# Kernel tuning notes

Hardware: AMD Instinct MI355X
Metric: run time of the kernel (lower is better)

The kernel has to match this reference:

```python
import jax, jax.numpy as jnp
import numpy as np
import math

B, S, E, H = 8, 1024, 512, 8
EPS = 1e-5

def _ln(x, g, b):
    mu = jnp.mean(x, axis=-1, keepdims=True)
    var = jnp.mean(jnp.square(x - mu), axis=-1, keepdims=True)
    return (x - mu) * jax.lax.rsqrt(var + EPS) * g + b

def setup_inputs() -> dict:
    key = jax.random.key(0)
    ks = iter(jax.random.split(key, 40))
    def w(shape, scale=0.02):
        return jax.random.normal(next(ks), shape, dtype=jnp.float32) * scale
    inp = {
        'x': jax.random.normal(next(ks), (B, S, E), dtype=jnp.float32),
        'cond': jax.random.normal(next(ks), (B, 1, E), dtype=jnp.float32),
        # AdaLN modulation linears (stored as (in,out))
        'g1w': w((E, E)), 'g1b': jnp.zeros((E,), jnp.float32),
        'be1w': w((E, E)), 'be1b': jnp.zeros((E,), jnp.float32),
        'a1w': w((E, E)), 'a1b': jnp.zeros((E,), jnp.float32),
        'g2w': w((E, E)), 'g2b': jnp.zeros((E,), jnp.float32),
        'be2w': w((E, E)), 'be2b': jnp.zeros((E,), jnp.float32),
        'a2w': w((E, E)), 'a2b': jnp.zeros((E,), jnp.float32),
        # LayerNorm affine
        'ln1g': jnp.ones((E,), jnp.float32), 'ln1b': jnp.zeros((E,), jnp.float32),
        'ln2g': jnp.ones((E,), jnp.float32), 'ln2b': jnp.zeros((E,), jnp.float32),
        # attention projections: each head has width E -> out dim H*E
        'wq': w((E, H * E)), 'bq': jnp.zeros((H * E,), jnp.float32),
        'wk': w((E, H * E)), 'bk': jnp.zeros((H * E,), jnp.float32),
        'wv': w((E, H * E)), 'bv': jnp.zeros((H * E,), jnp.float32),
        'lvw': w((H * E, E)), 'lvb': jnp.zeros((E,), jnp.float32),
        # FFN
        'f1w': w((E, 4 * E)), 'f1b': jnp.zeros((4 * E,), jnp.float32),
        'f2w': w((4 * E, E)), 'f2b': jnp.zeros((E,), jnp.float32),
    }
    return inp

def reference(x, cond, g1w, g1b, be1w, be1b, a1w, a1b, g2w, g2b, be2w, be2b, a2w, a2b,
              ln1g, ln1b, ln2g, ln2b, wq, bq, wk, bk, wv, bv, lvw, lvb, f1w, f1b, f2w, f2b):
    # AdaLN modulation signals, each (B,1,E)
    gamma1 = cond @ g1w + g1b
    beta1 = cond @ be1w + be1b
    alpha1 = cond @ a1w + a1b
    gamma2 = cond @ g2w + g2b
    beta2 = cond @ be2w + be2b
    alpha2 = cond @ a2w + a2b

    y = _ln(x, ln1g, ln1b) * (1.0 + gamma1) + beta1
    q = (y @ wq + bq).reshape(B, S, H, E).transpose(0, 2, 1, 3)  # (B,H,S,E)
    k = (y @ wk + bk).reshape(B, S, H, E).transpose(0, 2, 1, 3)
    v = (y @ wv + bv).reshape(B, S, H, E).transpose(0, 2, 1, 3)
    # NOTE: original scales by sqrt(q.size(2)) == sqrt(seq_len), not head_dim
    scale = 1.0 / math.sqrt(S)
    attn = jax.nn.softmax(jnp.einsum('bhse,bhte->bhst', q, k) * scale, axis=-1)
    o = jnp.einsum('bhst,bhte->bhse', attn, v)  # (B,H,S,E)
    o = o.transpose(0, 2, 1, 3).reshape(B, S, H * E)
    y = x + (o @ lvw + lvb) * alpha1

    z = _ln(y, ln2g, ln2b) * (1.0 + gamma2) + beta2
    z = (jax.nn.relu(z @ f1w + f1b) @ f2w + f2b) * alpha2
    return y + z
```

## Files before the change

kernel.cpp:

```cpp
#include <hip/hip_runtime.h>
#include <hip/hip_bf16.h>

typedef __bf16 bf16_t;
typedef bf16_t bf16x8 __attribute__((ext_vector_type(8)));
typedef bf16_t bf16x4 __attribute__((ext_vector_type(4)));
typedef float f32x4 __attribute__((ext_vector_type(4)));

typedef const __attribute__((address_space(1))) void GV;
typedef __attribute__((address_space(3))) void LV;

__device__ __forceinline__ void gload_lds16(const bf16_t* gsrc, bf16_t* ldst) {
    __builtin_amdgcn_global_load_lds((GV*)gsrc, (LV*)ldst, 16, 0, 0);
}

__global__ __launch_bounds__(256) void wtrans_all_kernel(
    const float* __restrict__ wq, const float* __restrict__ wk, const float* __restrict__ wv,
    const float* __restrict__ lvw, const float* __restrict__ f1w, const float* __restrict__ f2w,
    bf16_t* __restrict__ wqT, bf16_t* __restrict__ lvwT,
    bf16_t* __restrict__ f1wT, bf16_t* __restrict__ f2wT)
{
    __shared__ float tile[32][33];
    const int bid = blockIdx.x;
    const float* in; bf16_t* out; int K, N, nx, local;
    if (bid < 6144) {
        const int sec = bid >> 11;
        local = bid & 2047;
        in = (sec == 0) ? wq : ((sec == 1) ? wk : wv);
        out = wqT + (long long)sec * 2097152;
        K = 512; N = 4096; nx = 128;
    } else if (bid < 8192) {
        local = bid - 6144; in = lvw; out = lvwT; K = 4096; N = 512; nx = 16;
    } else if (bid < 9216) {
        local = bid - 8192; in = f1w; out = f1wT; K = 512; N = 2048; nx = 64;
    } else {
        local = bid - 9216; in = f2w; out = f2wT; K = 2048; N = 512; nx = 16;
    }
    const int n0 = (local % nx) * 32, k0 = (local / nx) * 32;
    const int tx = threadIdx.x & 31, ty = threadIdx.x >> 5;
#pragma unroll
    for (int i = 0; i < 32; i += 8)
        tile[ty + i][tx] = in[(long long)(k0 + ty + i) * N + n0 + tx];
    __syncthreads();
#pragma unroll
    for (int i = 0; i < 32; i += 8)
        out[(long long)(n0 + ty + i) * K + k0 + tx] = (bf16_t)tile[tx][ty + i];
}

__global__ __launch_bounds__(256) void modsig_kernel(
    const float* __restrict__ cond,
    const float* __restrict__ w0, const float* __restrict__ w1, const float* __restrict__ w2,
    const float* __restrict__ w3, const float* __restrict__ w4, const float* __restrict__ w5,
    const float* __restrict__ c0, const float* __restrict__ c1, const float* __restrict__ c2,
    const float* __restrict__ c3, const float* __restrict__ c4, const float* __restrict__ c5,
    float* __restrict__ out)
{
    __shared__ float cs[512];
    const int sig = blockIdx.x >> 3, b = blockIdx.x & 7;
    const float* w; const float* bi;
    switch (sig) {
        case 0: w = w0; bi = c0; break;
        case 1: w = w1; bi = c1; break;
        case 2: w = w2; bi = c2; break;
        case 3: w = w3; bi = c3; break;
        case 4: w = w4; bi = c4; break;
        default: w = w5; bi = c5; break;
    }
    for (int i = threadIdx.x; i < 512; i += 256) cs[i] = cond[b * 512 + i];
    __syncthreads();
    for (int n = threadIdx.x; n < 512; n += 256) {
        float s0 = 0.f, s1 = 0.f, s2 = 0.f, s3 = 0.f;
        for (int i = 0; i < 512; i += 4) {
            s0 = fmaf(cs[i], w[(long long)i * 512 + n], s0);
            s1 = fmaf(cs[i + 1], w[(long long)(i + 1) * 512 + n], s1);
            s2 = fmaf(cs[i + 2], w[(long long)(i + 2) * 512 + n], s2);
            s3 = fmaf(cs[i + 3], w[(long long)(i + 3) * 512 + n], s3);
        }
        out[(long long)(sig * 8 + b) * 512 + n] = bi[n] + (s0 + s1) + (s2 + s3);
    }
}

__global__ __launch_bounds__(128) void ln_mod_kernel(
    const float* __restrict__ x, const float* __restrict__ g, const float* __restrict__ be,
    const float* __restrict__ gamma, const float* __restrict__ beta, bf16_t* __restrict__ out)
{
    const int row = blockIdx.x;
    const int b = row >> 10;
    const int t = threadIdx.x;
    const float4 v = reinterpret_cast<const float4*>(x + (long long)row * 512)[t];
    float s = v.x + v.y + v.z + v.w;
    float ss = v.x * v.x + v.y * v.y + v.z * v.z + v.w * v.w;
    for (int o = 32; o; o >>= 1) { s += __shfl_xor(s, o); ss += __shfl_xor(ss, o); }
    __shared__ float red[4];
    if ((t & 63) == 0) { red[t >> 6] = s; red[2 + (t >> 6)] = ss; }
    __syncthreads();
    s = red[0] + red[1]; ss = red[2] + red[3];
    const float mu = s * (1.f / 512.f);
    const float rstd = rsqrtf(ss * (1.f / 512.f) - mu * mu + 1e-5f);
    const float4 gv = reinterpret_cast<const float4*>(g)[t];
    const float4 bv = reinterpret_cast<const float4*>(be)[t];
    const float4 ga = reinterpret_cast<const float4*>(gamma + b * 512)[t];
    const float4 bb = reinterpret_cast<const float4*>(beta + b * 512)[t];
    bf16x4 ov;
    ov[0] = (bf16_t)(((v.x - mu) * rstd * gv.x + bv.x) * (1.f + ga.x) + bb.x);
    ov[1] = (bf16_t)(((v.y - mu) * rstd * gv.y + bv.y) * (1.f + ga.y) + bb.y);
    ov[2] = (bf16_t)(((v.z - mu) * rstd * gv.z + bv.z) * (1.f + ga.z) + bb.z);
    ov[3] = (bf16_t)(((v.w - mu) * rstd * gv.w + bv.w) * (1.f + ga.w) + bb.w);
    reinterpret_cast<bf16x4*>(out + (long long)row * 512)[t] = ov;
}

template <int EPI>
__global__ __launch_bounds__(256) void gemm128_kernel(
    const bf16_t* __restrict__ A, const bf16_t* __restrict__ B,
    const float* __restrict__ bias, void* Cout,
    int M, int N, int K, int lda, int ldb, int ldc)
{
    const int nbx = gridDim.x;
    const int lin = blockIdx.y * nbx + blockIdx.x;
    const int cpx = (nbx * gridDim.y) >> 3;
    const int swz = (lin & 7) * cpx + (lin >> 3);
    const int m0 = (swz / nbx) * 128, n0 = (swz % nbx) * 128;
    const int tid = threadIdx.x, lane = tid & 63, wid = tid >> 6;
    const int wr = wid >> 1, wc = wid & 1;

    __shared__ bf16_t As[16384];
    __shared__ bf16_t Bs[16384];

    f32x4 acc[4][4];
#pragma unroll
    for (int m = 0; m < 4; ++m)
#pragma unroll
        for (int n = 0; n < 4; ++n) acc[m][n] = (f32x4){0.f, 0.f, 0.f, 0.f};

    const int r8 = lane >> 3;
    const int lc = (lane & 7) ^ r8;
    long long aOff[4], bOff[4];
#pragma unroll
    for (int i = 0; i < 4; ++i) {
        const int row = i * 32 + wid * 8 + r8;
        aOff[i] = (long long)(m0 + row) * lda + lc * 8;
        bOff[i] = (long long)(n0 + row) * ldb + lc * 8;
    }

    const int frow = lane & 15, lg = lane >> 4;
    const int p0 = lg ^ (frow & 7);

#pragma unroll
    for (int i = 0; i < 4; ++i) gload_lds16(A + aOff[i], As + i * 2048 + wid * 512);
#pragma unroll
    for (int i = 0; i < 4; ++i) gload_lds16(B + bOff[i], Bs + i * 2048 + wid * 512);

    for (int kt = 0; kt < K; kt += 64) {
        const int cur = (kt >> 6) & 1;
        __syncthreads();
        if (kt + 64 < K) {
            const int nxt = (cur ^ 1) * 8192;
#pragma unroll
            for (int i = 0; i < 4; ++i) gload_lds16(A + aOff[i] + kt + 64, As + nxt + i * 2048 + wid * 512);
#pragma unroll
            for (int i = 0; i < 4; ++i) gload_lds16(B + bOff[i] + kt + 64, Bs + nxt + i * 2048 + wid * 512);
        }
        const bf16_t* Ab = As + cur * 8192;
        const bf16_t* Bb = Bs + cur * 8192;
        __builtin_amdgcn_s_setprio(1);
#pragma unroll
        for (int kk = 0; kk < 2; ++kk) {
            const int pc = p0 ^ (kk << 2);
            bf16x8 af[4], bfv[4];
#pragma unroll
            for (int m = 0; m < 4; ++m)
                af[m] = *reinterpret_cast<const bf16x8*>(Ab + (wr * 64 + m * 16 + frow) * 64 + pc * 8);
#pragma unroll
            for (int n = 0; n < 4; ++n)
                bfv[n] = *reinterpret_cast<const bf16x8*>(Bb + (wc * 64 + n * 16 + frow) * 64 + pc * 8);
#pragma unroll
            for (int m = 0; m < 4; ++m)
#pragma unroll
                for (int n = 0; n < 4; ++n)
                    acc[m][n] = __builtin_amdgcn_mfma_f32_16x16x32_bf16(af[m], bfv[n], acc[m][n], 0, 0, 0);
        }
        __builtin_amdgcn_s_setprio(0);
    }

#pragma unroll
    for (int m = 0; m < 4; ++m) {
        const int gm = m0 + wr * 64 + m * 16 + ((lane >> 4) << 2);
#pragma unroll
        for (int n = 0; n < 4; ++n) {
            const int gn = n0 + wc * 64 + n * 16 + (lane & 15);
            const float bb = bias ? bias[gn] : 0.f;
#pragma unroll
            for (int j = 0; j < 4; ++j) {
                const float v = acc[m][n][j] + bb;
                const int gmj = gm + j;
                if (EPI == 0) {
                    ((bf16_t*)Cout)[(long long)gmj * ldc + gn] = (bf16_t)v;
                } else {
                    ((bf16_t*)Cout)[(long long)gmj * ldc + gn] = (bf16_t)fmaxf(v, 0.f);
                }
            }
        }
    }
}

__global__ __launch_bounds__(256) void gemmqkv_kernel(
    const bf16_t* __restrict__ A, const bf16_t* __restrict__ B,
    const float* __restrict__ bq, const float* __restrict__ bk, const float* __restrict__ bv,
    bf16_t* __restrict__ qkv, bf16_t* __restrict__ vtb)
{
    const int lin = blockIdx.y * 96 + blockIdx.x;
    const int swz = (lin & 7) * 768 + (lin >> 3);
    const int m0 = (swz / 96) * 128, n0 = (swz % 96) * 128;
    const int sec = n0 >> 12;
    const float* bias = (sec == 0) ? bq : ((sec == 1) ? bk : bv);
    const int tid = threadIdx.x, lane = tid & 63, wid = tid >> 6;
    const int wr = wid >> 1, wc = wid & 1;

    __shared__ bf16_t As[16384];
    __shared__ bf16_t Bs[16384];

    f32x4 acc[4][4];
#pragma unroll
    for (int m = 0; m < 4; ++m)
#pragma unroll
        for (int n = 0; n < 4; ++n) acc[m][n] = (f32x4){0.f, 0.f, 0.f, 0.f};

    const int r8 = lane >> 3;
    const int lc = (lane & 7) ^ r8;
    long long aOff[4], bOff[4];
#pragma unroll
    for (int i = 0; i < 4; ++i) {
        const int row = i * 32 + wid * 8 + r8;
        aOff[i] = (long long)(m0 + row) * 512 + lc * 8;
        bOff[i] = (long long)(n0 + row) * 512 + lc * 8;
    }

    const int frow = lane & 15, lg = lane >> 4;
    const int p0 = lg ^ (frow & 7);

#pragma unroll
    for (int i = 0; i < 4; ++i) gload_lds16(A + aOff[i], As + i * 2048 + wid * 512);
#pragma unroll
    for (int i = 0; i < 4; ++i) gload_lds16(B + bOff[i], Bs + i * 2048 + wid * 512);

    for (int kt = 0; kt < 512; kt += 64) {
        const int cur = (kt >> 6) & 1;
        __syncthreads();
        if (kt + 64 < 512) {
            const int nxt = (cur ^ 1) * 8192;
#pragma unroll
            for (int i = 0; i < 4; ++i) gload_lds16(A + aOff[i] + kt + 64, As + nxt + i * 2048 + wid * 512);
#pragma unroll
            for (int i = 0; i < 4; ++i) gload_lds16(B + bOff[i] + kt + 64, Bs + nxt + i * 2048 + wid * 512);
        }
        const bf16_t* Ab = As + cur * 8192;
        const bf16_t* Bb = Bs + cur * 8192;
        __builtin_amdgcn_s_setprio(1);
#pragma unroll
        for (int kk = 0; kk < 2; ++kk) {
            const int pc = p0 ^ (kk << 2);
            bf16x8 af[4], bfv[4];
#pragma unroll
            for (int m = 0; m < 4; ++m)
                af[m] = *reinterpret_cast<const bf16x8*>(Ab + (wr * 64 + m * 16 + frow) * 64 + pc * 8);
#pragma unroll
            for (int n = 0; n < 4; ++n)
                bfv[n] = *reinterpret_cast<const bf16x8*>(Bb + (wc * 64 + n * 16 + frow) * 64 + pc * 8);
#pragma unroll
            for (int m = 0; m < 4; ++m)
#pragma unroll
                for (int n = 0; n < 4; ++n)
                    acc[m][n] = __builtin_amdgcn_mfma_f32_16x16x32_bf16(af[m], bfv[n], acc[m][n], 0, 0, 0);
        }
        __builtin_amdgcn_s_setprio(0);
    }

#pragma unroll
    for (int m = 0; m < 4; ++m) {
        const int gm = m0 + wr * 64 + m * 16 + ((lane >> 4) << 2);
#pragma unroll
        for (int n = 0; n < 4; ++n) {
            const int gn = n0 + wc * 64 + n * 16 + (lane & 15);
            const int gnl = gn & 4095;
            const float bb = bias[gnl];
#pragma unroll
            for (int j = 0; j < 4; ++j) {
                const float v = acc[m][n][j] + bb;
                const int gmj = gm + j;
                if (sec < 2) {
                    qkv[(long long)sec * 33554432 + (long long)gmj * 4096 + gnl] = (bf16_t)v;
                } else {
                    const long long ci =
                        (long long)(((gmj >> 10) * 8 + (gnl >> 9)) * 512 + (gnl & 511)) * 1024 + (gmj & 1023);
                    vtb[ci] = (bf16_t)v;
                }
            }
        }
    }
}

__global__ __launch_bounds__(256) void gemm64_kernel(
    const bf16_t* __restrict__ A, const bf16_t* __restrict__ B,
    const float* __restrict__ bias, float* __restrict__ Cout,
    const float* __restrict__ resid, const float* __restrict__ alpha,
    int M, int N, int K, int lda, int ldb)
{
    const int nbx = gridDim.x;
    const int lin = blockIdx.y * nbx + blockIdx.x;
    const int cpx = (nbx * gridDim.y) >> 3;
    const int swz = (lin & 7) * cpx + (lin >> 3);
    const int m0 = (swz / nbx) * 64, n0 = (swz % nbx) * 128;
    const int tid = threadIdx.x, lane = tid & 63, wid = tid >> 6;
    const int wr = wid >> 1, wc = wid & 1;

    __shared__ bf16_t As[8192];
    __shared__ bf16_t Bs[16384];

    f32x4 acc[2][4];
#pragma unroll
    for (int m = 0; m < 2; ++m)
#pragma unroll
        for (int n = 0; n < 4; ++n) acc[m][n] = (f32x4){0.f, 0.f, 0.f, 0.f};

    const int r8 = lane >> 3;
    const int lc = (lane & 7) ^ r8;
    long long aOff[2], bOff[4];
#pragma unroll
    for (int i = 0; i < 2; ++i)
        aOff[i] = (long long)(m0 + i * 32 + wid * 8 + r8) * lda + lc * 8;
#pragma unroll
    for (int i = 0; i < 4; ++i)
        bOff[i] = (long long)(n0 + i * 32 + wid * 8 + r8) * ldb + lc * 8;

    const int frow = lane & 15, lg = lane >> 4;
    const int p0 = lg ^ (frow & 7);

#pragma unroll
    for (int i = 0; i < 2; ++i) gload_lds16(A + aOff[i], As + i * 2048 + wid * 512);
#pragma unroll
    for (int i = 0; i < 4; ++i) gload_lds16(B + bOff[i], Bs + i * 2048 + wid * 512);

    for (int kt = 0; kt < K; kt += 64) {
        const int cur = (kt >> 6) & 1;
        __syncthreads();
        if (kt + 64 < K) {
#pragma unroll
            for (int i = 0; i < 2; ++i)
                gload_lds16(A + aOff[i] + kt + 64, As + (cur ^ 1) * 4096 + i * 2048 + wid * 512);
#pragma unroll
            for (int i = 0; i < 4; ++i)
                gload_lds16(B + bOff[i] + kt + 64, Bs + (cur ^ 1) * 8192 + i * 2048 + wid * 512);
        }
        const bf16_t* Ab = As + cur * 4096;
        const bf16_t* Bb = Bs + cur * 8192;
        __builtin_amdgcn_s_setprio(1);
#pragma unroll
        for (int kk = 0; kk < 2; ++kk) {
            const int pc = p0 ^ (kk << 2);
            bf16x8 af[2], bfv[4];
#pragma unroll
            for (int m = 0; m < 2; ++m)
                af[m] = *reinterpret_cast<const bf16x8*>(Ab + (wr * 32 + m * 16 + frow) * 64 + pc * 8);
#pragma unroll
            for (int n = 0; n < 4; ++n)
                bfv[n] = *reinterpret_cast<const bf16x8*>(Bb + (wc * 64 + n * 16 + frow) * 64 + pc * 8);
#pragma unroll
            for (int m = 0; m < 2; ++m)
#pragma unroll
                for (int n = 0; n < 4; ++n)
                    acc[m][n] = __builtin_amdgcn_mfma_f32_16x16x32_bf16(af[m], bfv[n], acc[m][n], 0, 0, 0);
        }
        __builtin_amdgcn_s_setprio(0);
    }

#pragma unroll
    for (int m = 0; m < 2; ++m) {
        const int gm = m0 + wr * 32 + m * 16 + ((lane >> 4) << 2);
#pragma unroll
        for (int n = 0; n < 4; ++n) {
            const int gn = n0 + wc * 64 + n * 16 + (lane & 15);
            const float bb = bias[gn];
#pragma unroll
            for (int j = 0; j < 4; ++j) {
                const int gmj = gm + j;
                const long long ci = (long long)gmj * 512 + gn;
                Cout[ci] = resid[ci] + (acc[m][n][j] + bb) * alpha[(gmj >> 10) * 512 + gn];
            }
        }
    }
}

#define FA_LDS 68608
#define SCL 0.04508422132207354f
__global__ __launch_bounds__(256, 2) void flash_kernel(
    bf16_t* __restrict__ qb, const bf16_t* __restrict__ kb, const bf16_t* __restrict__ vtb)
{
    extern __shared__ char smem[];
    bf16_t* Ks = (bf16_t*)smem;
    bf16_t* Vs = (bf16_t*)(smem + 32768);
    char* PB = smem + 65536;
    float* pmaxB = (float*)(smem + 67584);
    float* psumB = (float*)(smem + 68096);

    const int bid = blockIdx.x;
    const int xcd = bid & 7, idx = bid >> 3;
    const int qt = idx & 31, bhl = idx >> 5;
    const int bh = xcd * 8 + bhl;
    const int b = bh >> 3, h = bh & 7;
    const int q0 = qt * 32;
    const int tid = threadIdx.x, lane = tid & 63, wid = tid >> 6;
    const int laneq = lane & 15, lx = lane & 7, lg = lane >> 4;
    const int wk = wid >> 1, wq = wid & 1;
    const int we = wid;

#pragma unroll
    for (int r = 0; r < 8; ++r) {
        const int row = r * 4 + wid;
        gload_lds16(kb + ((long long)(b * 1024 + row) * 8 + h) * 512 + ((lane ^ (row & 7)) << 3),
                    Ks + row * 512);
    }
    const int qi = wq * 16 + laneq;
    bf16x8 qfrag[16];
    {
        const bf16_t* qrow = qb + ((long long)(b * 1024 + q0 + qi) * 8 + h) * 512 + lg * 8;
#pragma unroll
        for (int ks = 0; ks < 16; ++ks) qfrag[ks] = *reinterpret_cast<const bf16x8*>(qrow + ks * 32);
    }
    f32x4 accA[8], accB[8];
#pragma unroll
    for (int e = 0; e < 8; ++e) { accA[e] = (f32x4){0.f,0.f,0.f,0.f}; accB[e] = (f32x4){0.f,0.f,0.f,0.f}; }
    float mS = 0.f, mPA = 0.f, mPB = 0.f, lA = 0.f, lB = 0.f;
    const int rA = wk * 16 + laneq;
    const int qA = laneq, qB = laneq + 16;
    __syncthreads();

    for (int t = 0; t < 32; ++t) {
#pragma unroll
        for (int r = 0; r < 8; ++r) {
            const int e0 = (r * 4 + wid) * 16;
            const int e = e0 + (lane >> 2);
            gload_lds16(vtb + ((long long)bh * 512 + e) * 1024 + t * 32 + (((lane & 3) ^ (e & 3)) << 3),
                        Vs + e0 * 32);
        }
        f32x4 s0 = (f32x4){0.f, 0.f, 0.f, 0.f};
        const char* KsB = (const char*)Ks;
        __builtin_amdgcn_s_setprio(1);
#pragma unroll
        for (int ks = 0; ks < 16; ++ks) {
            const int co = (((ks * 4 + lg) ^ lx) << 4);
            bf16x8 a0 = *(const bf16x8*)(KsB + rA * 1024 + co);
            s0 = __builtin_amdgcn_mfma_f32_16x16x32_bf16(a0, qfrag[ks], s0, 0, 0, 0);
        }
        __builtin_amdgcn_s_setprio(0);
        float f[4], pe[4];
#pragma unroll
        for (int j = 0; j < 4; ++j) f[j] = s0[j] * SCL;
        float mloc = fmaxf(fmaxf(f[0], f[1]), fmaxf(f[2], f[3]));
        mloc = fmaxf(mloc, __shfl_xor(mloc, 16));
        mloc = fmaxf(mloc, __shfl_xor(mloc, 32));
        float sl = 0.f;
#pragma unroll
        for (int j = 0; j < 4; ++j) { pe[j] = exp2f(f[j] - mS); sl += pe[j]; }
        sl += __shfl_xor(sl, 16);
        sl += __shfl_xor(sl, 32);
        if (lane < 16) {
            pmaxB[(t & 1) * 64 + wk * 32 + wq * 16 + lane] = mloc;
            psumB[(t & 1) * 64 + wk * 32 + wq * 16 + lane] = sl;
        }
        {
            bf16x4 p;
#pragma unroll
            for (int j = 0; j < 4; ++j) p[j] = (bf16_t)pe[j];
            const int g = wk * 4 + lg;
            *(bf16x4*)(PB + qi * 64 + (((g >> 1) ^ (qi & 3)) << 4) + ((g & 1) << 3)) = p;
        }
        __syncthreads();

        if (t < 31) {
#pragma unroll
            for (int r = 0; r < 8; ++r) {
                const int row = r * 4 + wid;
                gload_lds16(kb + ((long long)(b * 1024 + t * 32 + 32 + row) * 8 + h) * 512
                                + ((lane ^ (row & 7)) << 3),
                            Ks + row * 512);
            }
        }
        const char* VB = (const char*)Vs;
        bf16x8 pA = *(const bf16x8*)(PB + qA * 64 + ((lg ^ (qA & 3)) << 4));
        bf16x8 pBv = *(const bf16x8*)(PB + qB * 64 + ((lg ^ (qB & 3)) << 4));
        __builtin_amdgcn_s_setprio(1);
#pragma unroll
        for (int ef = 0; ef < 8; ++ef) {
            const int re = we * 128 + ef * 16 + laneq;
            bf16x8 av = *(const bf16x8*)(VB + re * 64 + ((lg ^ (re & 3)) << 4));
            accA[ef] = __builtin_amdgcn_mfma_f32_16x16x32_bf16(av, pA, accA[ef], 0, 0, 0);
            accB[ef] = __builtin_amdgcn_mfma_f32_16x16x32_bf16(av, pBv, accB[ef], 0, 0, 0);
        }
        __builtin_amdgcn_s_setprio(0);
        {
            const float* pmax_t = pmaxB + (t & 1) * 64;
            const float* psum_t = psumB + (t & 1) * 64;
            mS = fmaxf(mS, fmaxf(pmax_t[qi], pmax_t[32 + qi]));
            lA += psum_t[qA] + psum_t[32 + qA];
            lB += psum_t[qB] + psum_t[32 + qB];
            const float mnA = fmaxf(mPA, fmaxf(pmax_t[qA], pmax_t[32 + qA]));
            const float mnB = fmaxf(mPB, fmaxf(pmax_t[qB], pmax_t[32 + qB]));
            if (__ballot((mnA > mPA) || (mnB > mPB))) {
                const float rsA = exp2f(mPA - mnA), rsB = exp2f(mPB - mnB);
                lA *= rsA; lB *= rsB;
#pragma unroll
                for (int e = 0; e < 8; ++e) {
#pragma unroll
                    for (int j = 0; j < 4; ++j) { accA[e][j] *= rsA; accB[e][j] *= rsB; }
                }
            }
            mPA = mnA; mPB = mnB;
        }
        __syncthreads();
    }

    const float iA = 1.f / lA, iB = 1.f / lB;
#pragma unroll
    for (int ef = 0; ef < 8; ++ef) {
        const int e0 = we * 128 + ef * 16 + lg * 4;
        bf16x4 oA, oB;
#pragma unroll
        for (int j = 0; j < 4; ++j) { oA[j] = (bf16_t)(accA[ef][j] * iA); oB[j] = (bf16_t)(accB[ef][j] * iB); }
        *(bf16x4*)(qb + ((long long)(b * 1024 + q0 + qA) * 8 + h) * 512 + e0) = oA;
        *(bf16x4*)(qb + ((long long)(b * 1024 + q0 + qB) * 8 + h) * 512 + e0) = oB;
    }
}

extern "C" void kernel_launch(void* const* d_in, const int* in_sizes, int n_in,
                              void* d_out, int out_size, void* d_ws, size_t ws_size,
                              hipStream_t stream)
{
    const float* x    = (const float*)d_in[0];
    const float* cond = (const float*)d_in[1];
    const float* g1w  = (const float*)d_in[2];  const float* g1b  = (const float*)d_in[3];
    const float* be1w = (const float*)d_in[4];  const float* be1b = (const float*)d_in[5];
    const float* a1w  = (const float*)d_in[6];  const float* a1b  = (const float*)d_in[7];
    const float* g2w  = (const float*)d_in[8];  const float* g2b  = (const float*)d_in[9];
    const float* be2w = (const float*)d_in[10]; const float* be2b = (const float*)d_in[11];
    const float* a2w  = (const float*)d_in[12]; const float* a2b  = (const float*)d_in[13];
    const float* ln1g = (const float*)d_in[14]; const float* ln1b = (const float*)d_in[15];
    const float* ln2g = (const float*)d_in[16]; const float* ln2b = (const float*)d_in[17];
    const float* wq   = (const float*)d_in[18]; const float* bq   = (const float*)d_in[19];
    const float* wk   = (const float*)d_in[20]; const float* bk   = (const float*)d_in[21];
    const float* wv   = (const float*)d_in[22]; const float* bv   = (const float*)d_in[23];
    const float* lvw  = (const float*)d_in[24]; const float* lvb  = (const float*)d_in[25];
    const float* f1w  = (const float*)d_in[26]; const float* f1b  = (const float*)d_in[27];
    const float* f2w  = (const float*)d_in[28]; const float* f2b  = (const float*)d_in[29];
    (void)in_sizes; (void)n_in; (void)out_size; (void)ws_size;

    char* w8 = (char*)d_ws;
    float*  mod  = (float*)(w8);
    bf16_t* wqT  = (bf16_t*)(w8 + 98304);
    bf16_t* lvwT = (bf16_t*)(w8 + 98304 + 3 * 4194304);
    bf16_t* f1wT = (bf16_t*)(w8 + 98304 + 4 * 4194304);
    bf16_t* f2wT = (bf16_t*)(w8 + 98304 + 4 * 4194304 + 2097152);
    bf16_t* ybf  = (bf16_t*)(w8 + 98304 + 4 * 4194304 + 2 * 2097152);
    bf16_t* qb   = (bf16_t*)(w8 + 98304 + 4 * 4194304 + 2 * 2097152 + 8388608);
    bf16_t* kb   = qb + 33554432;
    bf16_t* vtb  = kb + 33554432;

    (void)hipFuncSetAttribute((const void*)flash_kernel,
                              hipFuncAttributeMaxDynamicSharedMemorySize, FA_LDS);

    const dim3 blk(256);
    wtrans_all_kernel<<<10240, blk, 0, stream>>>(wq, wk, wv, lvw, f1w, f2w,
                                                 wqT, lvwT, f1wT, f2wT);
    modsig_kernel<<<48, blk, 0, stream>>>(cond, g1w, be1w, a1w, g2w, be2w, a2w,
                                          g1b, be1b, a1b, g2b, be2b, a2b, mod);
    ln_mod_kernel<<<8192, 128, 0, stream>>>(x, ln1g, ln1b, mod, mod + 4096, ybf);
    gemmqkv_kernel<<<dim3(96, 64), blk, 0, stream>>>(ybf, wqT, bq, bk, bv, qb, vtb);
    flash_kernel<<<2048, 256, FA_LDS, stream>>>(qb, kb, vtb);
    gemm64_kernel<<<dim3(4, 128), blk, 0, stream>>>(qb, lvwT, lvb, (float*)d_out, x, mod + 8192,
        8192, 512, 4096, 4096, 4096);
    ln_mod_kernel<<<8192, 128, 0, stream>>>((const float*)d_out, ln2g, ln2b,
                                            mod + 12288, mod + 16384, ybf);
    gemm128_kernel<1><<<dim3(16, 64), blk, 0, stream>>>(ybf, f1wT, f1b, qb,
        8192, 2048, 512, 512, 512, 2048);
    gemm64_kernel<<<dim3(4, 128), blk, 0, stream>>>(qb, f2wT, f2b, (float*)d_out,
        (const float*)d_out, mod + 20480,
        8192, 512, 2048, 2048, 2048);
}
```

Before: 678.9 us.

## Merge weight transpose and modulation kernels; reswizzle flash attention LDS layouts

Folds the AdaLN modulation-signal matmul into the weight-transpose kernel as 48 extra blocks, removing one launch. In the flash kernel it changes the XOR swizzle for the V and P tiles in LDS to key on (row>>1)&3 instead of row&3, to reduce bank conflicts on 64-byte rows. It also interleaves the per-row max and sum partials so each row's two partials are read with one float2 load. The partial buffers grow LDS use by 1 KB, which may affect occupancy at two blocks per CU.

```diff
diff --git a/kernel.cpp b/kernel.cpp
--- a/kernel.cpp
+++ b/kernel.cpp
@@ -13,69 +13,70 @@
     __builtin_amdgcn_global_load_lds((GV*)gsrc, (LV*)ldst, 16, 0, 0);
 }
 
-__global__ __launch_bounds__(256) void wtrans_all_kernel(
+__global__ __launch_bounds__(256) void prep_kernel(
     const float* __restrict__ wq, const float* __restrict__ wk, const float* __restrict__ wv,
     const float* __restrict__ lvw, const float* __restrict__ f1w, const float* __restrict__ f2w,
     bf16_t* __restrict__ wqT, bf16_t* __restrict__ lvwT,
-    bf16_t* __restrict__ f1wT, bf16_t* __restrict__ f2wT)
-{
-    __shared__ float tile[32][33];
+    bf16_t* __restrict__ f1wT, bf16_t* __restrict__ f2wT,
+    const float* __restrict__ cond,
+    const float* __restrict__ mw0, const float* __restrict__ mw1, const float* __restrict__ mw2,
+    const float* __restrict__ mw3, const float* __restrict__ mw4, const float* __restrict__ mw5,
+    const float* __restrict__ mc0, const float* __restrict__ mc1, const float* __restrict__ mc2,
+    const float* __restrict__ mc3, const float* __restrict__ mc4, const float* __restrict__ mc5,
+    float* __restrict__ mod)
+{
+    __shared__ float sbuf[32 * 33];
     const int bid = blockIdx.x;
-    const float* in; bf16_t* out; int K, N, nx, local;
-    if (bid < 6144) {
-        const int sec = bid >> 11;
-        local = bid & 2047;
-        in = (sec == 0) ? wq : ((sec == 1) ? wk : wv);
-        out = wqT + (long long)sec * 2097152;
-        K = 512; N = 4096; nx = 128;
-    } else if (bid < 8192) {
-        local = bid - 6144; in = lvw; out = lvwT; K = 4096; N = 512; nx = 16;
-    } else if (bid < 9216) {
-        local = bid - 8192; in = f1w; out = f1wT; K = 512; N = 2048; nx = 64;
+    if (bid < 10240) {
+        float (*tile)[33] = (float(*)[33])sbuf;
+        const float* in; bf16_t* out; int N, nx, K, local;
+        if (bid < 6144) {
+            const int sec = bid >> 11;
+            local = bid & 2047;
+            in = (sec == 0) ? wq : ((sec == 1) ? wk : wv);
+            out = wqT + (long long)sec * 2097152;
+            K = 512; N = 4096; nx = 128;
+        } else if (bid < 8192) {
+            local = bid - 6144; in = lvw; out = lvwT; K = 4096; N = 512; nx = 16;
+        } else if (bid < 9216) {
+            local = bid - 8192; in = f1w; out = f1wT; K = 512; N = 2048; nx = 64;
+        } else {
+            local = bid - 9216; in = f2w; out = f2wT; K = 2048; N = 512; nx = 16;
+        }
+        const int n0 = (local % nx) * 32, k0 = (local / nx) * 32;
+        const int tx = threadIdx.x & 31, ty = threadIdx.x >> 5;
+#pragma unroll
+        for (int i = 0; i < 32; i += 8)
+            tile[ty + i][tx] = in[(long long)(k0 + ty + i) * N + n0 + tx];
+        __syncthreads();
+#pragma unroll
+        for (int i = 0; i < 32; i += 8)
+            out[(long long)(n0 + ty + i) * K + k0 + tx] = (bf16_t)tile[tx][ty + i];
     } else {
-        local = bid - 9216; in = f2w; out = f2wT; K = 2048; N = 512; nx = 16;
-    }
-    const int n0 = (local % nx) * 32, k0 = (local / nx) * 32;
-    const int tx = threadIdx.x & 31, ty = threadIdx.x >> 5;
-#pragma unroll
-    for (int i = 0; i < 32; i += 8)
-        tile[ty + i][tx] = in[(long long)(k0 + ty + i) * N + n0 + tx];
-    __syncthreads();
-#pragma unroll
-    for (int i = 0; i < 32; i += 8)
-        out[(long long)(n0 + ty + i) * K + k0 + tx] = (bf16_t)tile[tx][ty + i];
-}
-
-__global__ __launch_bounds__(256) void modsig_kernel(
-    const float* __restrict__ cond,
-    const float* __restrict__ w0, const float* __restrict__ w1, const float* __restrict__ w2,
-    const float* __restrict__ w3, const float* __restrict__ w4, const float* __restrict__ w5,
-    const float* __restrict__ c0, const float* __restrict__ c1, const float* __restrict__ c2,
-    const float* __restrict__ c3, const float* __restrict__ c4, const float* __restrict__ c5,
-    float* __restrict__ out)
-{
-    __shared__ float cs[512];
-    const int sig = blockIdx.x >> 3, b = blockIdx.x & 7;
-    const float* w; const float* bi;
-    switch (sig) {
-        case 0: w = w0; bi = c0; break;
-        case 1: w = w1; bi = c1; break;
-        case 2: w = w2; bi = c2; break;
-        case 3: w = w3; bi = c3; break;
-        case 4: w = w4; bi = c4; break;
-        default: w = w5; bi = c5; break;
-    }
-    for (int i = threadIdx.x; i < 512; i += 256) cs[i] = cond[b * 512 + i];
-    __syncthreads();
-    for (int n = threadIdx.x; n < 512; n += 256) {
-        float s0 = 0.f, s1 = 0.f, s2 = 0.f, s3 = 0.f;
-        for (int i = 0; i < 512; i += 4) {
-            s0 = fmaf(cs[i], w[(long long)i * 512 + n], s0);
-            s1 = fmaf(cs[i + 1], w[(long long)(i + 1) * 512 + n], s1);
-            s2 = fmaf(cs[i + 2], w[(long long)(i + 2) * 512 + n], s2);
-            s3 = fmaf(cs[i + 3], w[(long long)(i + 3) * 512 + n], s3);
-        }
-        out[(long long)(sig * 8 + b) * 512 + n] = bi[n] + (s0 + s1) + (s2 + s3);
+        float* cs = sbuf;
+        const int lb = bid - 10240;
+        const int sig = lb >> 3, b = lb & 7;
+        const float* w; const float* bi;
+        switch (sig) {
+            case 0: w = mw0; bi = mc0; break;
+            case 1: w = mw1; bi = mc1; break;
+            case 2: w = mw2; bi = mc2; break;
+            case 3: w = mw3; bi = mc3; break;
+            case 4: w = mw4; bi = mc4; break;
+            default: w = mw5; bi = mc5; break;
+        }
+        for (int i = threadIdx.x; i < 512; i += 256) cs[i] = cond[b * 512 + i];
+        __syncthreads();
+        for (int n = threadIdx.x; n < 512; n += 256) {
+            float s0 = 0.f, s1 = 0.f, s2 = 0.f, s3 = 0.f;
+            for (int i = 0; i < 512; i += 4) {
+                s0 = fmaf(cs[i], w[(long long)i * 512 + n], s0);
+                s1 = fmaf(cs[i + 1], w[(long long)(i + 1) * 512 + n], s1);
+                s2 = fmaf(cs[i + 2], w[(long long)(i + 2) * 512 + n], s2);
+                s3 = fmaf(cs[i + 3], w[(long long)(i + 3) * 512 + n], s3);
+            }
+            mod[(long long)(sig * 8 + b) * 512 + n] = bi[n] + (s0 + s1) + (s2 + s3);
+        }
     }
 }
 
@@ -389,7 +390,7 @@
     }
 }
 
-#define FA_LDS 68608
+#define FA_LDS 69632
 #define SCL 0.04508422132207354f
 __global__ __launch_bounds__(256, 2) void flash_kernel(
     bf16_t* __restrict__ qb, const bf16_t* __restrict__ kb, const bf16_t* __restrict__ vtb)
@@ -399,7 +400,7 @@
     bf16_t* Vs = (bf16_t*)(smem + 32768);
     char* PB = smem + 65536;
     float* pmaxB = (float*)(smem + 67584);
-    float* psumB = (float*)(smem + 68096);
+    float* psumB = (float*)(smem + 68608);
 
     const int bid = blockIdx.x;
     const int xcd = bid & 7, idx = bid >> 3;
@@ -438,7 +439,8 @@
         for (int r = 0; r < 8; ++r) {
             const int e0 = (r * 4 + wid) * 16;
             const int e = e0 + (lane >> 2);
-            gload_lds16(vtb + ((long long)bh * 512 + e) * 1024 + t * 32 + (((lane & 3) ^ (e & 3)) << 3),
+            gload_lds16(vtb + ((long long)bh * 512 + e) * 1024 + t * 32
+                            + (((lane & 3) ^ ((e >> 1) & 3)) << 3),
                         Vs + e0 * 32);
         }
         f32x4 s0 = (f32x4){0.f, 0.f, 0.f, 0.f};
@@ -463,15 +465,16 @@
         sl += __shfl_xor(sl, 16);
         sl += __shfl_xor(sl, 32);
         if (lane < 16) {
-            pmaxB[(t & 1) * 64 + wk * 32 + wq * 16 + lane] = mloc;
-            psumB[(t & 1) * 64 + wk * 32 + wq * 16 + lane] = sl;
+            const int si = (t & 1) * 64 + (wq * 16 + lane) * 2 + wk;
+            pmaxB[si] = mloc;
+            psumB[si] = sl;
         }
         {
             bf16x4 p;
 #pragma unroll
             for (int j = 0; j < 4; ++j) p[j] = (bf16_t)pe[j];
             const int g = wk * 4 + lg;
-            *(bf16x4*)(PB + qi * 64 + (((g >> 1) ^ (qi & 3)) << 4) + ((g & 1) << 3)) = p;
+            *(bf16x4*)(PB + qi * 64 + ((((g >> 1) ^ ((qi >> 1) & 3))) << 4) + ((g & 1) << 3)) = p;
         }
         __syncthreads();
 
@@ -485,13 +488,13 @@
             }
         }
         const char* VB = (const char*)Vs;
-        bf16x8 pA = *(const bf16x8*)(PB + qA * 64 + ((lg ^ (qA & 3)) << 4));
-        bf16x8 pBv = *(const bf16x8*)(PB + qB * 64 + ((lg ^ (qB & 3)) << 4));
+        bf16x8 pA = *(const bf16x8*)(PB + qA * 64 + ((lg ^ ((qA >> 1) & 3)) << 4));
+        bf16x8 pBv = *(const bf16x8*)(PB + qB * 64 + ((lg ^ ((qB >> 1) & 3)) << 4));
         __builtin_amdgcn_s_setprio(1);
 #pragma unroll
         for (int ef = 0; ef < 8; ++ef) {
             const int re = we * 128 + ef * 16 + laneq;
-            bf16x8 av = *(const bf16x8*)(VB + re * 64 + ((lg ^ (re & 3)) << 4));
+            bf16x8 av = *(const bf16x8*)(VB + re * 64 + ((lg ^ ((re >> 1) & 3)) << 4));
             accA[ef] = __builtin_amdgcn_mfma_f32_16x16x32_bf16(av, pA, accA[ef], 0, 0, 0);
             accB[ef] = __builtin_amdgcn_mfma_f32_16x16x32_bf16(av, pBv, accB[ef], 0, 0, 0);
         }
@@ -499,11 +502,15 @@
         {
             const float* pmax_t = pmaxB + (t & 1) * 64;
             const float* psum_t = psumB + (t & 1) * 64;
-            mS = fmaxf(mS, fmaxf(pmax_t[qi], pmax_t[32 + qi]));
-            lA += psum_t[qA] + psum_t[32 + qA];
-            lB += psum_t[qB] + psum_t[32 + qB];
-            const float mnA = fmaxf(mPA, fmaxf(pmax_t[qA], pmax_t[32 + qA]));
-            const float mnB = fmaxf(mPB, fmaxf(pmax_t[qB], pmax_t[32 + qB]));
+            const float2 pmA = *(const float2*)&pmax_t[qA * 2];
+            const float2 pmB = *(const float2*)&pmax_t[qB * 2];
+            const float2 psA = *(const float2*)&psum_t[qA * 2];
+            const float2 psB = *(const float2*)&psum_t[qB * 2];
+            mS = fmaxf(mS, wq ? fmaxf(pmB.x, pmB.y) : fmaxf(pmA.x, pmA.y));
+            lA += psA.x + psA.y;
+            lB += psB.x + psB.y;
+            const float mnA = fmaxf(mPA, fmaxf(pmA.x, pmA.y));
+            const float mnB = fmaxf(mPB, fmaxf(pmB.x, pmB.y));
             if (__ballot((mnA > mPA) || (mnB > mPB))) {
                 const float rsA = exp2f(mPA - mnA), rsB = exp2f(mPB - mnB);
                 lA *= rsA; lB *= rsB;
@@ -567,10 +574,10 @@
                               hipFuncAttributeMaxDynamicSharedMemorySize, FA_LDS);
 
     const dim3 blk(256);
-    wtrans_all_kernel<<<10240, blk, 0, stream>>>(wq, wk, wv, lvw, f1w, f2w,
-                                                 wqT, lvwT, f1wT, f2wT);
-    modsig_kernel<<<48, blk, 0, stream>>>(cond, g1w, be1w, a1w, g2w, be2w, a2w,
-                                          g1b, be1b, a1b, g2b, be2b, a2b, mod);
+    prep_kernel<<<10288, blk, 0, stream>>>(wq, wk, wv, lvw, f1w, f2w,
+                                           wqT, lvwT, f1wT, f2wT,
+                                           cond, g1w, be1w, a1w, g2w, be2w, a2w,
+                                           g1b, be1b, a1b, g2b, be2b, a2b, mod);
     ln_mod_kernel<<<8192, 128, 0, stream>>>(x, ln1g, ln1b, mod, mod + 4096, ybf);
     gemmqkv_kernel<<<dim3(96, 64), blk, 0, stream>>>(ybf, wqT, bq, bk, bv, qb, vtb);
     flash_kernel<<<2048, 256, FA_LDS, stream>>>(qb, kb, vtb);
```

Result: no change. 673.9 us (-0.7%).
